# Optimization experiments

Hardware: AMD Instinct MI355X
Metric: run time of the kernel (lower is better)

## Reference

```python
import jax, jax.numpy as jnp
import numpy as np

# --- config (matches init_kwargs) ---
H = 16          # num_attention_heads
DH = 64         # size_per_head
U = H * DH      # units = 1024
M = 8           # num_memory_slots
L = M + 1       # memory slots + current input row
R = 2 * M + 1   # relative position range
EPS = 1e-6
FORGET_BIAS = 1.0
INPUT_BIAS = 0.0
SCALE = 1.0 / np.sqrt(DH)


def _rel_emb():
    # sinusoidal relative-position embedding table [2M+1, U]
    p = np.arange(-M, M + 1, dtype=np.float64)
    i = np.arange(U)
    expo = np.where(i % 2 == 0, i, i - 1) / U
    ang = p[:, None] / np.power(10000.0, expo)[None, :]
    tab = np.where(i % 2 == 0, np.sin(ang), np.cos(ang))
    return jnp.asarray(tab, dtype=jnp.float32)

REL_EMB = _rel_emb()
# rel index table: idx[q,k] = q - k + M  (replaces one-hot pos_table matmul)
_qi = jnp.arange(L)
REL_IDX = _qi[:, None] - _qi[None, :] + M  # [L, L]


def _hard_sigmoid(x):
    return jnp.clip(0.2 * x + 0.5, 0.0, 1.0)


def _ln(x, g, b):
    m = jnp.mean(x, axis=-1, keepdims=True)
    v = jnp.var(x, axis=-1, keepdims=True)
    return (x - m) * jax.lax.rsqrt(v + EPS) * g + b


def setup_inputs() -> dict:
    key = jax.random.key(0)
    ks = jax.random.split(key, 12)
    B, T, DIN = 32, 128, 1024
    s = 0.02
    return {
        "x": jax.random.normal(ks[0], (B, T, DIN), jnp.float32),
        "input_kernel": jax.random.normal(ks[1], (DIN, U), jnp.float32) * s,
        "input_bias": jnp.zeros((U,), jnp.float32),
        "gate_kernel": jax.random.normal(ks[2], (DIN, 2 * U), jnp.float32) * s,
        "recurrent_kernel": jax.random.normal(ks[3], (U, 2 * U), jnp.float32) * s,
        "recurrent_bias": jnp.zeros((2 * U,), jnp.float32),
        "attention_kernel": jax.random.normal(ks[4], (U, 3 * U), jnp.float32) * s,
        "attention_bias": jnp.zeros((3 * U,), jnp.float32),
        "mlp_kernel": jax.random.normal(ks[5], (U, 2 * U), jnp.float32) * s,
        "mlp_bias": jnp.zeros((2 * U,), jnp.float32),
        "ln_gamma": jnp.ones((2 * U,), jnp.float32),
        "ln_beta": jnp.zeros((2 * U,), jnp.float32),
        "rel_kernel": jax.random.normal(ks[6], (U, U), jnp.float32) * s,
    }


def _forward(x, input_kernel, input_bias, gate_kernel, recurrent_kernel,
             recurrent_bias, attention_kernel, attention_bias, mlp_kernel,
             mlp_bias, ln_gamma, ln_beta, rel_kernel):
    B = x.shape[0]
    # relative key projection, shared across steps: [R, H, DH]
    r = (REL_EMB @ rel_kernel).reshape(R, H, DH)

    def step(mem, xt):
        # xt: [B, DIN]; mem: [B, M, U]
        xp = xt @ input_kernel + input_bias              # [B, U]
        mp = jnp.concatenate([mem, xp[:, None, :]], axis=1)  # [B, L, U]
        qkv = mp @ attention_kernel + attention_bias     # [B, L, 3U]
        q, k, v = jnp.split(qkv, 3, axis=-1)
        q = q.reshape(B, L, H, DH).transpose(0, 2, 1, 3)  # [B,H,L,DH]
        k = k.reshape(B, L, H, DH).transpose(0, 2, 1, 3)
        v = v.reshape(B, L, H, DH).transpose(0, 2, 1, 3)
        scores = jnp.einsum('bhqd,bhkd->bhqk', q, k) * SCALE
        rsc = jnp.einsum('bhqd,rhd->bhqr', q, r) * SCALE  # [B,H,L,R]
        scores = scores + rsc[:, :, jnp.arange(L)[:, None], REL_IDX]
        p = jax.nn.softmax(scores, axis=-1)
        attn = jnp.einsum('bhqk,bhkd->bhqd', p, v)
        attn = attn.transpose(0, 2, 1, 3).reshape(B, L, U)
        a1 = _ln(mp + attn, ln_gamma[:U], ln_beta[:U])
        h = jax.nn.gelu(a1 @ mlp_kernel[:, :U] + mlp_bias[:U])
        m2 = h @ mlp_kernel[:, U:] + mlp_bias[U:]
        cand = _ln(a1 + m2, ln_gamma[U:], ln_beta[U:])
        # LSTM-style per-slot gating
        g = (xt @ gate_kernel)[:, None, :] + mp @ recurrent_kernel + recurrent_bias
        ig, fg = jnp.split(g, 2, axis=-1)
        ig = _hard_sigmoid(ig + INPUT_BIAS)
        fg = _hard_sigmoid(fg + FORGET_BIAS)
        nmp = fg * mp + ig * jnp.tanh(cand)              # [B, L, U]
        return nmp[:, :M, :], nmp[:, -1, :]

    mem0 = jnp.zeros((B, M, U), x.dtype)
    _, ys = jax.lax.scan(step, mem0, x.transpose(1, 0, 2))
    return ys.transpose(1, 0, 2)  # [B, T, U]


def reference(x, input_kernel, input_bias, gate_kernel, recurrent_kernel,
              recurrent_bias, attention_kernel, attention_bias, mlp_kernel,
              mlp_bias, ln_gamma, ln_beta, rel_kernel):
    return _forward(x, input_kernel, input_bias, gate_kernel, recurrent_kernel,
                    recurrent_bias, attention_kernel, attention_bias,
                    mlp_kernel, mlp_bias, ln_gamma, ln_beta, rel_kernel)
```

## Files before the change

### kernel.cpp

```cpp
#include <hip/hip_runtime.h>
#include <hip/hip_bf16.h>
#include <math.h>

#define BB 32
#define TT 128
#define UU 1024
#define MM 8
#define LL 9
#define RR 17
#define MROWS 288
#define RSC 4096.0f
#define RSCI (1.0f/4096.0f)

typedef _Float16 f16x8 __attribute__((ext_vector_type(8)));
typedef float f32x4 __attribute__((ext_vector_type(4)));
typedef float f32x8 __attribute__((ext_vector_type(8)));

__device__ __forceinline__ void split2(float v, _Float16* h1, _Float16* h2)
{
    _Float16 a = (_Float16)v;
    float r = (v - (float)a) * RSC;
    *h1 = a; *h2 = (_Float16)r;
}

__device__ __forceinline__ void split2x8(const f32x8 v, f16x8& a, f16x8& b)
{
#pragma unroll
    for (int j = 0; j < 8; ++j) {
        float f = v[j];
        _Float16 h1 = (_Float16)f;
        float r = (f - (float)h1) * RSC;
        a[j] = h1; b[j] = (_Float16)r;
    }
}

__device__ __forceinline__ float gelu_f(float x)
{
    float t = tanhf(0.7978845608028654f * (x + 0.044715f * x * x * x));
    return 0.5f * x * (1.f + t);
}

template<int CG, int NKS, int KLEN>
__global__ __launch_bounds__(256) void gemmks(
    const float* __restrict__ A,
    const _Float16* __restrict__ B1, const _Float16* __restrict__ B2,
    float* __restrict__ P, int N, int GdivP)
{
    static_assert(KLEN % 128 == 0, "pipeline processes chunk pairs");
    int tid = threadIdx.x, wave = tid >> 6, lane = tid & 63;
    int bid = blockIdx.x;
    int x = bid & 7, inner = bid >> 3;
    int q = inner % GdivP, rowT = inner / GdivP;
    int g = x + 8 * q;
    int colT = g / NKS, ks = g % NKS;

    int lr = lane & 15, kg = lane >> 4;
    int row0 = rowT * 32 + (wave & 1) * 16;
    int col0 = colT * (CG * 32) + (wave >> 1) * (CG * 16);
    int kbase = ks * KLEN;

    const float* Ap = A + (size_t)(row0 + lr) * 1024 + kbase + kg * 8;
    size_t boff = (size_t)(col0 + lr) * 1024 + kbase + kg * 8;

    f32x4 accM[CG], accR[CG];
#pragma unroll
    for (int c = 0; c < CG; ++c) {
        accM[c] = (f32x4){0.f, 0.f, 0.f, 0.f};
        accR[c] = (f32x4){0.f, 0.f, 0.f, 0.f};
    }

    f32x8 afA0, afA1, afB0, afB1;
    f16x8 bvA[2][CG][2], bvB[2][CG][2];

    auto loadChunkA = [&](int kc) {
        afA0 = *(const f32x8*)(Ap + kc);
        afA1 = *(const f32x8*)(Ap + kc + 32);
#pragma unroll
        for (int h = 0; h < 2; ++h)
#pragma unroll
            for (int c = 0; c < CG; ++c) {
                size_t o = boff + (size_t)c * 16 * 1024 + kc + h * 32;
                bvA[h][c][0] = *(const f16x8*)(B1 + o);
                bvA[h][c][1] = *(const f16x8*)(B2 + o);
            }
    };
    auto loadChunkB = [&](int kc) {
        afB0 = *(const f32x8*)(Ap + kc);
        afB1 = *(const f32x8*)(Ap + kc + 32);
#pragma unroll
        for (int h = 0; h < 2; ++h)
#pragma unroll
            for (int c = 0; c < CG; ++c) {
                size_t o = boff + (size_t)c * 16 * 1024 + kc + h * 32;
                bvB[h][c][0] = *(const f16x8*)(B1 + o);
                bvB[h][c][1] = *(const f16x8*)(B2 + o);
            }
    };
    auto mfmaChunkA = [&]() {
#pragma unroll
        for (int h = 0; h < 2; ++h) {
            f16x8 a1, a2s;
            split2x8(h ? afA1 : afA0, a1, a2s);
#pragma unroll
            for (int c = 0; c < CG; ++c) {
                accM[c] = __builtin_amdgcn_mfma_f32_16x16x32_f16(a1, bvA[h][c][0], accM[c], 0, 0, 0);
                accR[c] = __builtin_amdgcn_mfma_f32_16x16x32_f16(a1, bvA[h][c][1], accR[c], 0, 0, 0);
                accR[c] = __builtin_amdgcn_mfma_f32_16x16x32_f16(a2s, bvA[h][c][0], accR[c], 0, 0, 0);
            }
        }
    };
    auto mfmaChunkB = [&]() {
#pragma unroll
        for (int h = 0; h < 2; ++h) {
            f16x8 a1, a2s;
            split2x8(h ? afB1 : afB0, a1, a2s);
#pragma unroll
            for (int c = 0; c < CG; ++c) {
                accM[c] = __builtin_amdgcn_mfma_f32_16x16x32_f16(a1, bvB[h][c][0], accM[c], 0, 0, 0);
                accR[c] = __builtin_amdgcn_mfma_f32_16x16x32_f16(a1, bvB[h][c][1], accR[c], 0, 0, 0);
                accR[c] = __builtin_amdgcn_mfma_f32_16x16x32_f16(a2s, bvB[h][c][0], accR[c], 0, 0, 0);
            }
        }
    };

    loadChunkA(0);
#pragma unroll
    for (int kc = 0; kc < KLEN; kc += 128) {
        loadChunkB(kc + 64);
        mfmaChunkA();
        if (kc + 128 < KLEN) loadChunkA(kc + 128);
        mfmaChunkB();
    }

    int r0 = row0 + kg * 4;
    float* Pk = P + (size_t)ks * MROWS * N;
#pragma unroll
    for (int c = 0; c < CG; ++c) {
        int col = col0 + c * 16 + lr;
#pragma unroll
        for (int r = 0; r < 4; ++r)
            Pk[(size_t)(r0 + r) * N + col] = accM[c][r] + accR[c][r] * RSCI;
    }
}

__global__ __launch_bounds__(256) void add4(
    const float* __restrict__ P, const float* __restrict__ bias,
    float* __restrict__ out, int N, int act, int total4)
{
    int idx = blockIdx.x * 256 + threadIdx.x;
    if (idx >= total4) return;
    size_t e = (size_t)idx * 4;
    size_t SP = (size_t)MROWS * N;
    int col = (int)(e % N);
    f32x4 p0 = *(const f32x4*)(P + e);
    f32x4 p1 = *(const f32x4*)(P + SP + e);
    f32x4 p2 = *(const f32x4*)(P + 2 * SP + e);
    f32x4 p3 = *(const f32x4*)(P + 3 * SP + e);
    f32x4 bv = *(const f32x4*)(bias + col);
    f32x4 s;
#pragma unroll
    for (int j = 0; j < 4; ++j) {
        float v = ((p0[j] + p1[j]) + (p2[j] + p3[j])) + bv[j];
        s[j] = act ? gelu_f(v) : v;
    }
    *(f32x4*)(out + e) = s;
}

__global__ __launch_bounds__(256) void gemm2(
    const float* __restrict__ A,
    const _Float16* __restrict__ B1, const _Float16* __restrict__ B2,
    const float* __restrict__ bias, float* __restrict__ C, int ldc, int act)
{
    int wave = threadIdx.x >> 6, lane = threadIdx.x & 63;
    int row0 = blockIdx.y * 32 + (wave >> 1) * 16;
    int col0 = blockIdx.x * 128 + (wave & 1) * 64;
    int lr = lane & 15, kofs = (lane >> 4) * 8;
    const float* Ap = A + (size_t)(row0 + lr) * 1024 + kofs;
    size_t boff = (size_t)(col0 + lr) * 1024 + kofs;
    f32x4 accM[4], accR[4];
#pragma unroll
    for (int c = 0; c < 4; ++c) {
        accM[c] = (f32x4){0.f, 0.f, 0.f, 0.f};
        accR[c] = (f32x4){0.f, 0.f, 0.f, 0.f};
    }
    for (int k = 0; k < 1024; k += 32) {
        f32x8 af = *(const f32x8*)(Ap + k);
        f16x8 a1, a2s;
        split2x8(af, a1, a2s);
#pragma unroll
        for (int c = 0; c < 4; ++c) {
            size_t o = boff + (size_t)c * 16 * 1024 + k;
            f16x8 b1 = *(const f16x8*)(B1 + o);
            f16x8 b2 = *(const f16x8*)(B2 + o);
            accM[c] = __builtin_amdgcn_mfma_f32_16x16x32_f16(a1, b1, accM[c], 0, 0, 0);
            accR[c] = __builtin_amdgcn_mfma_f32_16x16x32_f16(a1, b2, accR[c], 0, 0, 0);
            accR[c] = __builtin_amdgcn_mfma_f32_16x16x32_f16(a2s, b1, accR[c], 0, 0, 0);
        }
    }
    int r0 = row0 + (lane >> 4) * 4;
#pragma unroll
    for (int c = 0; c < 4; ++c) {
        int col = col0 + c * 16 + lr;
        float bv = bias ? bias[col] : 0.f;
#pragma unroll
        for (int r = 0; r < 4; ++r) {
            float v = accM[c][r] + accR[c][r] * RSCI + bv;
            if (act == 1) v = gelu_f(v);
            C[(size_t)(r0 + r) * ldc + col] = v;
        }
    }
}

__global__ __launch_bounds__(256) void transpose_split(
    const float* __restrict__ in,
    _Float16* __restrict__ o1, _Float16* __restrict__ o2, int N)
{
    __shared__ float t[32][33];
    int tx = threadIdx.x & 31, ty = threadIdx.x >> 5;
    int k0 = blockIdx.y * 32, n0 = blockIdx.x * 32;
#pragma unroll
    for (int i = 0; i < 4; ++i)
        t[ty + i * 8][tx] = in[(size_t)(k0 + ty + i * 8) * N + n0 + tx];
    __syncthreads();
#pragma unroll
    for (int i = 0; i < 4; ++i) {
        float v = t[tx][ty + i * 8];
        size_t off = (size_t)(n0 + ty + i * 8) * 1024 + k0 + tx;
        split2(v, o1 + off, o2 + off);
    }
}

#define BKK 16
__global__ __launch_bounds__(256) void gemm_f32(
    const float* __restrict__ A, const float* __restrict__ B,
    float* __restrict__ C, int M, int N, int K)
{
    __shared__ float As[BKK][65];
    __shared__ float Bs[BKK][64];
    int tid = threadIdx.x;
    int row0 = blockIdx.y * 64, col0 = blockIdx.x * 64;
    int ty = tid >> 4, tx = tid & 15;
    float acc[4][4];
#pragma unroll
    for (int i = 0; i < 4; ++i)
#pragma unroll
        for (int j = 0; j < 4; ++j) acc[i][j] = 0.f;
    for (int k0 = 0; k0 < K; k0 += BKK) {
        {
            int r = tid >> 2, kv = (tid & 3) * 4;
            float4 v = make_float4(0.f, 0.f, 0.f, 0.f);
            int gr = row0 + r;
            if (gr < M) v = *(const float4*)(A + (size_t)gr * K + k0 + kv);
            As[kv + 0][r] = v.x; As[kv + 1][r] = v.y;
            As[kv + 2][r] = v.z; As[kv + 3][r] = v.w;
        }
        {
            int r = tid >> 4, cv = (tid & 15) * 4;
            float4 v = *(const float4*)(B + (size_t)(k0 + r) * N + col0 + cv);
            *(float4*)&Bs[r][cv] = v;
        }
        __syncthreads();
#pragma unroll
        for (int kk = 0; kk < BKK; ++kk) {
            float a[4], b[4];
#pragma unroll
            for (int j = 0; j < 4; ++j) a[j] = As[kk][ty * 4 + j];
#pragma unroll
            for (int j = 0; j < 4; ++j) b[j] = Bs[kk][tx * 4 + j];
#pragma unroll
            for (int i = 0; i < 4; ++i)
#pragma unroll
                for (int j = 0; j < 4; ++j) acc[i][j] += a[i] * b[j];
        }
        __syncthreads();
    }
#pragma unroll
    for (int i = 0; i < 4; ++i) {
        int gr = row0 + ty * 4 + i;
        if (gr >= M) continue;
#pragma unroll
        for (int j = 0; j < 4; ++j)
            C[(size_t)gr * N + col0 + tx * 4 + j] = acc[i][j];
    }
}

__global__ void relemb_kernel(float* __restrict__ tab)
{
    int p = blockIdx.x;
    float pv = (float)(p - MM);
    for (int i = threadIdx.x; i < UU; i += blockDim.x) {
        float expo = (float)(i & ~1) * (1.0f / (float)UU);
        float scale = exp2f(-expo * 13.287712379549449f);
        float ang = pv * scale;
        tab[p * UU + i] = (i & 1) ? cosf(ang) : sinf(ang);
    }
}

__global__ void init_mp(const float* __restrict__ xp_all, float* __restrict__ mp)
{
    int row = blockIdx.x;
    int b = row / LL, l = row % LL;
    for (int u = threadIdx.x; u < UU; u += blockDim.x)
        mp[(size_t)row * UU + u] = (l == MM) ? xp_all[((size_t)b * TT) * UU + u] : 0.f;
}

__global__ __launch_bounds__(512) void attn_ln(
    const float* __restrict__ qkvg, const float* __restrict__ rproj,
    const float* __restrict__ mp,
    const float* __restrict__ gamma, const float* __restrict__ beta,
    float* __restrict__ a1)
{
    __shared__ float sA[LL][UU];
    __shared__ float red[16];
    int b = blockIdx.x;
    int tid = threadIdx.x;
    int wave = tid >> 6, lane = tid & 63;

    for (int hh = 0; hh < 2; ++hh) {
        int h = wave + hh * 8;
        const float* base = qkvg + (size_t)b * LL * 5120 + h * 64 + lane;
        float q[LL], k[LL], v[LL], r[RR];
#pragma unroll
        for (int l = 0; l < LL; ++l) {
            q[l] = base[l * 5120];
            k[l] = base[l * 5120 + 1024];
            v[l] = base[l * 5120 + 2048];
        }
#pragma unroll
        for (int rp = 0; rp < RR; ++rp) r[rp] = rproj[rp * UU + h * 64 + lane];
#pragma unroll
        for (int qr = 0; qr < LL; ++qr) {
            float sc[LL];
#pragma unroll
            for (int kr = 0; kr < LL; ++kr) {
                float prod = q[qr] * (k[kr] + r[qr - kr + MM]);
#pragma unroll
                for (int o = 32; o > 0; o >>= 1) prod += __shfl_xor(prod, o);
                sc[kr] = prod * 0.125f;
            }
            float m = sc[0];
#pragma unroll
            for (int kr = 1; kr < LL; ++kr) m = fmaxf(m, sc[kr]);
            float s = 0.f;
#pragma unroll
            for (int kr = 0; kr < LL; ++kr) { sc[kr] = expf(sc[kr] - m); s += sc[kr]; }
            float inv = 1.0f / s;
            float acc = 0.f;
#pragma unroll
            for (int kr = 0; kr < LL; ++kr) acc += sc[kr] * v[kr];
            sA[qr][h * 64 + lane] = acc * inv;
        }
    }
    __syncthreads();

    for (int l = 0; l < LL; ++l) {
        size_t row = (size_t)(b * LL + l);
        float x0 = mp[row * UU + tid] + sA[l][tid];
        float x1 = mp[row * UU + tid + 512] + sA[l][tid + 512];
        float s = x0 + x1, ss = x0 * x0 + x1 * x1;
#pragma unroll
        for (int o = 32; o > 0; o >>= 1) { s += __shfl_xor(s, o); ss += __shfl_xor(ss, o); }
        if (lane == 0) { red[wave * 2] = s; red[wave * 2 + 1] = ss; }
        __syncthreads();
        float S = 0.f, SS = 0.f;
#pragma unroll
        for (int w = 0; w < 8; ++w) { S += red[w * 2]; SS += red[w * 2 + 1]; }
        __syncthreads();
        float mean = S * (1.0f / UU);
        float var = SS * (1.0f / UU) - mean * mean;
        float rstd = rsqrtf(var + 1e-6f);
        a1[row * UU + tid]       = (x0 - mean) * rstd * gamma[tid] + beta[tid];
        a1[row * UU + tid + 512] = (x1 - mean) * rstd * gamma[tid + 512] + beta[tid + 512];
    }
}

__global__ __launch_bounds__(256) void finalize_step(
    const float* __restrict__ a1, const float* __restrict__ m2P,
    const float* __restrict__ bm,
    const float* __restrict__ qkvg, const float* __restrict__ gx_all,
    const float* __restrict__ xp_all,
    const float* __restrict__ gamma, const float* __restrict__ beta,
    float* __restrict__ mp, float* __restrict__ out, int t)
{
    __shared__ float red[8];
    int row = blockIdx.x;
    int b = row / LL, l = row % LL;
    int tid = threadIdx.x;
    int wave = tid >> 6, lane = tid & 63;
    const size_t SP = (size_t)MROWS * UU;

    float x[4];
    float s = 0.f, ss = 0.f;
#pragma unroll
    for (int j = 0; j < 4; ++j) {
        int u = tid + j * 256;
        size_t off = (size_t)row * UU + u;
        float m2v = ((m2P[off] + m2P[SP + off]) + (m2P[2 * SP + off] + m2P[3 * SP + off]))
                    + bm[1024 + u];
        x[j] = a1[off] + m2v;
        s += x[j]; ss += x[j] * x[j];
    }
#pragma unroll
    for (int o = 32; o > 0; o >>= 1) { s += __shfl_xor(s, o); ss += __shfl_xor(ss, o); }
    if (lane == 0) { red[wave * 2] = s; red[wave * 2 + 1] = ss; }
    __syncthreads();
    float S = 0.f, SS = 0.f;
#pragma unroll
    for (int w = 0; w < 4; ++w) { S += red[w * 2]; SS += red[w * 2 + 1]; }
    float mean = S * (1.0f / UU);
    float rstd = rsqrtf(SS * (1.0f / UU) - mean * mean + 1e-6f);

    size_t gxoff = ((size_t)b * TT + t) * 2048;
    size_t grow = (size_t)row * 5120 + 3072;
#pragma unroll
    for (int j = 0; j < 4; ++j) {
        int u = tid + j * 256;
        float cand = (x[j] - mean) * rstd * gamma[1024 + u] + beta[1024 + u];
        float tc = tanhf(cand);
        float gi = gx_all[gxoff + u]        + qkvg[grow + u];
        float gf = gx_all[gxoff + 1024 + u] + qkvg[grow + 1024 + u];
        float ig = fminf(fmaxf(0.2f * gi + 0.5f, 0.f), 1.f);
        float fg = fminf(fmaxf(0.2f * (gf + 1.0f) + 0.5f, 0.f), 1.f);
        size_t off = (size_t)row * UU + u;
        float nmp = fg * mp[off] + ig * tc;
        if (l < MM) {
            mp[off] = nmp;
        } else {
            out[((size_t)b * TT + t) * UU + u] = nmp;
            if (t + 1 < TT)
                mp[off] = xp_all[((size_t)b * TT + t + 1) * UU + u];
        }
    }
}

extern "C" void kernel_launch(void* const* d_in, const int* in_sizes, int n_in,
                              void* d_out, int out_size, void* d_ws, size_t ws_size,
                              hipStream_t stream)
{
    const float* x    = (const float*)d_in[0];
    const float* Wi   = (const float*)d_in[1];
    const float* bi   = (const float*)d_in[2];
    const float* Wg   = (const float*)d_in[3];
    const float* Wr   = (const float*)d_in[4];
    const float* br   = (const float*)d_in[5];
    const float* Wa   = (const float*)d_in[6];
    const float* ba   = (const float*)d_in[7];
    const float* Wm   = (const float*)d_in[8];
    const float* bm   = (const float*)d_in[9];
    const float* gam  = (const float*)d_in[10];
    const float* bet  = (const float*)d_in[11];
    const float* Wrel = (const float*)d_in[12];
    float* out = (float*)d_out;

    char* w = (char*)d_ws;
    float*  xp_all = (float*)w;  w += (size_t)BB*TT*UU*4;
    float*  gx_all = (float*)w;  w += (size_t)BB*TT*2048*4;
    size_t W1N = (size_t)5120 * 1024, WMN = (size_t)2048 * 1024;
    _Float16* W1a = (_Float16*)w;  w += W1N*2;
    _Float16* W1b = (_Float16*)w;  w += W1N*2;
    _Float16* Wma = (_Float16*)w;  w += WMN*2;
    _Float16* Wmb = (_Float16*)w;  w += WMN*2;
    float*  b1    = (float*)w;   w += 5120*4;
    float*  tab   = (float*)w;   w += RR*UU*4;
    float*  rproj = (float*)w;   w += RR*UU*4;
    float*  mp    = (float*)w;   w += (size_t)MROWS*UU*4;
    float*  qkvg  = (float*)w;   w += (size_t)MROWS*5120*4;
    float*  a1    = (float*)w;   w += (size_t)MROWS*UU*4;
    float*  hbuf  = (float*)w;   w += (size_t)MROWS*UU*4;
    char* sbase = w;
    float*  qkvgP = (float*)w;   w += (size_t)4*MROWS*5120*4;
    float*  m1P   = (float*)w;   w += (size_t)4*MROWS*UU*4;
    float*  m2P   = (float*)w;   w += (size_t)4*MROWS*UU*4;
    _Float16* Wia = (_Float16*)sbase;
    _Float16* Wib = Wia + (size_t)1024 * 1024;
    _Float16* Wga = Wib + (size_t)1024 * 1024;
    _Float16* Wgb = Wga + (size_t)2048 * 1024;

    relemb_kernel<<<RR, 256, 0, stream>>>(tab);
    gemm_f32<<<dim3(UU / 64, 1), 256, 0, stream>>>(tab, Wrel, rproj, RR, UU, UU);
    transpose_split<<<dim3(3072 / 32, 32), 256, 0, stream>>>(Wa, W1a, W1b, 3072);
    transpose_split<<<dim3(2048 / 32, 32), 256, 0, stream>>>(
        Wr, W1a + (size_t)3072 * 1024, W1b + (size_t)3072 * 1024, 2048);
    transpose_split<<<dim3(2048 / 32, 32), 256, 0, stream>>>(Wm, Wma, Wmb, 2048);
    transpose_split<<<dim3(1024 / 32, 32), 256, 0, stream>>>(Wi, Wia, Wib, 1024);
    transpose_split<<<dim3(2048 / 32, 32), 256, 0, stream>>>(Wg, Wga, Wgb, 2048);
    hipMemcpyAsync(b1, ba, 3072 * sizeof(float), hipMemcpyDeviceToDevice, stream);
    hipMemcpyAsync(b1 + 3072, br, 2048 * sizeof(float), hipMemcpyDeviceToDevice, stream);
    gemm2<<<dim3(UU / 128, (BB * TT) / 32), 256, 0, stream>>>(
        x, Wia, Wib, bi, xp_all, UU, 0);
    gemm2<<<dim3(2048 / 128, (BB * TT) / 32), 256, 0, stream>>>(
        x, Wga, Wgb, nullptr, gx_all, 2048, 0);
    init_mp<<<MROWS, 256, 0, stream>>>(xp_all, mp);

    for (int t = 0; t < TT; ++t) {
        gemmks<2, 4, 256><<<2880, 256, 0, stream>>>(mp, W1a, W1b, qkvgP, 5120, 40);
        add4<<<(MROWS * 5120 / 4 + 255) / 256, 256, 0, stream>>>(
            qkvgP, b1, qkvg, 5120, 0, MROWS * 5120 / 4);
        attn_ln<<<BB, 512, 0, stream>>>(qkvg, rproj, mp, gam, bet, a1);
        gemmks<2, 4, 256><<<576, 256, 0, stream>>>(a1, Wma, Wmb, m1P, UU, 8);
        add4<<<(MROWS * UU / 4 + 255) / 256, 256, 0, stream>>>(
            m1P, bm, hbuf, UU, 1, MROWS * UU / 4);
        gemmks<2, 4, 256><<<576, 256, 0, stream>>>(hbuf, Wma + (size_t)1024 * 1024,
                                                   Wmb + (size_t)1024 * 1024, m2P, UU, 8);
        finalize_step<<<MROWS, 256, 0, stream>>>(a1, m2P, bm, qkvg, gx_all, xp_all,
                                                 gam, bet, mp, out, t);
    }
}
```

Before: 20.95 ms.

## Fuse split-K reduction and GELU into second MLP GEMM; trim qkv reduction

New measurement: 22.78 ms. 1.09x slower.

```diff
diff --git a/kernel.cpp b/kernel.cpp
--- a/kernel.cpp
+++ b/kernel.cpp
@@ -143,27 +143,106 @@
     }
 }
 
-__global__ __launch_bounds__(256) void add4(
+template<int CG, int NKS, int KLEN>
+__global__ __launch_bounds__(256) void gemmks_af(
+    const float* __restrict__ A,
+    const _Float16* __restrict__ B1, const _Float16* __restrict__ B2,
+    const float* __restrict__ abias,
+    float* __restrict__ P, int N, int GdivP)
+{
+    int tid = threadIdx.x, wave = tid >> 6, lane = tid & 63;
+    int bid = blockIdx.x;
+    int x = bid & 7, inner = bid >> 3;
+    int q = inner % GdivP, rowT = inner / GdivP;
+    int g = x + 8 * q;
+    int colT = g / NKS, ks = g % NKS;
+
+    int lr = lane & 15, kg = lane >> 4;
+    int row0 = rowT * 32 + (wave & 1) * 16;
+    int col0 = colT * (CG * 32) + (wave >> 1) * (CG * 16);
+    int kbase = ks * KLEN;
+
+    const float* Ap = A + (size_t)(row0 + lr) * 1024 + kbase + kg * 8;
+    const float* bp = abias + kbase + kg * 8;
+    const size_t SPA = (size_t)MROWS * 1024;
+    size_t boff = (size_t)(col0 + lr) * 1024 + kbase + kg * 8;
+
+    f32x4 accM[CG], accR[CG];
+#pragma unroll
+    for (int c = 0; c < CG; ++c) {
+        accM[c] = (f32x4){0.f, 0.f, 0.f, 0.f};
+        accR[c] = (f32x4){0.f, 0.f, 0.f, 0.f};
+    }
+
+    for (int kc = 0; kc < KLEN; kc += 64) {
+        f32x8 p00 = *(const f32x8*)(Ap + kc);
+        f32x8 p01 = *(const f32x8*)(Ap + SPA + kc);
+        f32x8 p02 = *(const f32x8*)(Ap + 2 * SPA + kc);
+        f32x8 p03 = *(const f32x8*)(Ap + 3 * SPA + kc);
+        f32x8 p10 = *(const f32x8*)(Ap + kc + 32);
+        f32x8 p11 = *(const f32x8*)(Ap + SPA + kc + 32);
+        f32x8 p12 = *(const f32x8*)(Ap + 2 * SPA + kc + 32);
+        f32x8 p13 = *(const f32x8*)(Ap + 3 * SPA + kc + 32);
+        f32x8 bv0 = *(const f32x8*)(bp + kc);
+        f32x8 bv1 = *(const f32x8*)(bp + kc + 32);
+        f32x8 af0, af1;
+#pragma unroll
+        for (int j = 0; j < 8; ++j) {
+            af0[j] = gelu_f(((p00[j] + p01[j]) + (p02[j] + p03[j])) + bv0[j]);
+            af1[j] = gelu_f(((p10[j] + p11[j]) + (p12[j] + p13[j])) + bv1[j]);
+        }
+        f16x8 bv[2][CG][2];
+#pragma unroll
+        for (int h = 0; h < 2; ++h)
+#pragma unroll
+            for (int c = 0; c < CG; ++c) {
+                size_t o = boff + (size_t)c * 16 * 1024 + kc + h * 32;
+                bv[h][c][0] = *(const f16x8*)(B1 + o);
+                bv[h][c][1] = *(const f16x8*)(B2 + o);
+            }
+#pragma unroll
+        for (int h = 0; h < 2; ++h) {
+            f16x8 a1, a2s;
+            split2x8(h ? af1 : af0, a1, a2s);
+#pragma unroll
+            for (int c = 0; c < CG; ++c) {
+                accM[c] = __builtin_amdgcn_mfma_f32_16x16x32_f16(a1, bv[h][c][0], accM[c], 0, 0, 0);
+                accR[c] = __builtin_amdgcn_mfma_f32_16x16x32_f16(a1, bv[h][c][1], accR[c], 0, 0, 0);
+                accR[c] = __builtin_amdgcn_mfma_f32_16x16x32_f16(a2s, bv[h][c][0], accR[c], 0, 0, 0);
+            }
+        }
+    }
+
+    int r0 = row0 + kg * 4;
+    float* Pk = P + (size_t)ks * MROWS * N;
+#pragma unroll
+    for (int c = 0; c < CG; ++c) {
+        int col = col0 + c * 16 + lr;
+#pragma unroll
+        for (int r = 0; r < 4; ++r)
+            Pk[(size_t)(r0 + r) * N + col] = accM[c][r] + accR[c][r] * RSCI;
+    }
+}
+
+__global__ __launch_bounds__(256) void add4q(
     const float* __restrict__ P, const float* __restrict__ bias,
-    float* __restrict__ out, int N, int act, int total4)
+    float* __restrict__ out)
 {
     int idx = blockIdx.x * 256 + threadIdx.x;
-    if (idx >= total4) return;
-    size_t e = (size_t)idx * 4;
-    size_t SP = (size_t)MROWS * N;
-    int col = (int)(e % N);
+    if (idx >= MROWS * 3072 / 4) return;
+    int row = idx / 768, cq = (idx % 768) * 4;
+    size_t SP = (size_t)MROWS * 5120;
+    size_t e = (size_t)row * 5120 + cq;
     f32x4 p0 = *(const f32x4*)(P + e);
     f32x4 p1 = *(const f32x4*)(P + SP + e);
     f32x4 p2 = *(const f32x4*)(P + 2 * SP + e);
     f32x4 p3 = *(const f32x4*)(P + 3 * SP + e);
-    f32x4 bv = *(const f32x4*)(bias + col);
+    f32x4 bv = *(const f32x4*)(bias + cq);
     f32x4 s;
 #pragma unroll
-    for (int j = 0; j < 4; ++j) {
-        float v = ((p0[j] + p1[j]) + (p2[j] + p3[j])) + bv[j];
-        s[j] = act ? gelu_f(v) : v;
-    }
-    *(f32x4*)(out + e) = s;
+    for (int j = 0; j < 4; ++j)
+        s[j] = ((p0[j] + p1[j]) + (p2[j] + p3[j])) + bv[j];
+    *(f32x4*)(out + (size_t)row * 3072 + cq) = s;
 }
 
 __global__ __launch_bounds__(256) void gemm2(
@@ -305,7 +384,7 @@
 }
 
 __global__ __launch_bounds__(512) void attn_ln(
-    const float* __restrict__ qkvg, const float* __restrict__ rproj,
+    const float* __restrict__ qkvgC, const float* __restrict__ rproj,
     const float* __restrict__ mp,
     const float* __restrict__ gamma, const float* __restrict__ beta,
     float* __restrict__ a1)
@@ -318,13 +397,13 @@
 
     for (int hh = 0; hh < 2; ++hh) {
         int h = wave + hh * 8;
-        const float* base = qkvg + (size_t)b * LL * 5120 + h * 64 + lane;
+        const float* base = qkvgC + (size_t)b * LL * 3072 + h * 64 + lane;
         float q[LL], k[LL], v[LL], r[RR];
 #pragma unroll
         for (int l = 0; l < LL; ++l) {
-            q[l] = base[l * 5120];
-            k[l] = base[l * 5120 + 1024];
-            v[l] = base[l * 5120 + 2048];
+            q[l] = base[l * 3072];
+            k[l] = base[l * 3072 + 1024];
+            v[l] = base[l * 3072 + 2048];
         }
 #pragma unroll
         for (int rp = 0; rp < RR; ++rp) r[rp] = rproj[rp * UU + h * 64 + lane];
@@ -377,7 +456,8 @@
 __global__ __launch_bounds__(256) void finalize_step(
     const float* __restrict__ a1, const float* __restrict__ m2P,
     const float* __restrict__ bm,
-    const float* __restrict__ qkvg, const float* __restrict__ gx_all,
+    const float* __restrict__ qkvgP, const float* __restrict__ b1,
+    const float* __restrict__ gx_all,
     const float* __restrict__ xp_all,
     const float* __restrict__ gamma, const float* __restrict__ beta,
     float* __restrict__ mp, float* __restrict__ out, int t)
@@ -388,6 +468,7 @@
     int tid = threadIdx.x;
     int wave = tid >> 6, lane = tid & 63;
     const size_t SP = (size_t)MROWS * UU;
+    const size_t SPA = (size_t)MROWS * 5120;
 
     float x[4];
     float s = 0.f, ss = 0.f;
@@ -417,8 +498,14 @@
         int u = tid + j * 256;
         float cand = (x[j] - mean) * rstd * gamma[1024 + u] + beta[1024 + u];
         float tc = tanhf(cand);
-        float gi = gx_all[gxoff + u]        + qkvg[grow + u];
-        float gf = gx_all[gxoff + 1024 + u] + qkvg[grow + 1024 + u];
+        float qgi = ((qkvgP[grow + u] + qkvgP[SPA + grow + u])
+                     + (qkvgP[2 * SPA + grow + u] + qkvgP[3 * SPA + grow + u]))
+                    + b1[3072 + u];
+        float qgf = ((qkvgP[grow + 1024 + u] + qkvgP[SPA + grow + 1024 + u])
+                     + (qkvgP[2 * SPA + grow + 1024 + u] + qkvgP[3 * SPA + grow + 1024 + u]))
+                    + b1[4096 + u];
+        float gi = gx_all[gxoff + u]        + qgi;
+        float gf = gx_all[gxoff + 1024 + u] + qgf;
         float ig = fminf(fmaxf(0.2f * gi + 0.5f, 0.f), 1.f);
         float fg = fminf(fmaxf(0.2f * (gf + 1.0f) + 0.5f, 0.f), 1.f);
         size_t off = (size_t)row * UU + u;
@@ -464,9 +551,8 @@
     float*  tab   = (float*)w;   w += RR*UU*4;
     float*  rproj = (float*)w;   w += RR*UU*4;
     float*  mp    = (float*)w;   w += (size_t)MROWS*UU*4;
-    float*  qkvg  = (float*)w;   w += (size_t)MROWS*5120*4;
     float*  a1    = (float*)w;   w += (size_t)MROWS*UU*4;
-    float*  hbuf  = (float*)w;   w += (size_t)MROWS*UU*4;
+    float*  qkvgC = (float*)w;   w += (size_t)MROWS*3072*4;
     char* sbase = w;
     float*  qkvgP = (float*)w;   w += (size_t)4*MROWS*5120*4;
     float*  m1P   = (float*)w;   w += (size_t)4*MROWS*UU*4;
@@ -494,15 +580,13 @@
 
     for (int t = 0; t < TT; ++t) {
         gemmks<2, 4, 256><<<2880, 256, 0, stream>>>(mp, W1a, W1b, qkvgP, 5120, 40);
-        add4<<<(MROWS * 5120 / 4 + 255) / 256, 256, 0, stream>>>(
-            qkvgP, b1, qkvg, 5120, 0, MROWS * 5120 / 4);
-        attn_ln<<<BB, 512, 0, stream>>>(qkvg, rproj, mp, gam, bet, a1);
+        add4q<<<864, 256, 0, stream>>>(qkvgP, b1, qkvgC);
+        attn_ln<<<BB, 512, 0, stream>>>(qkvgC, rproj, mp, gam, bet, a1);
         gemmks<2, 4, 256><<<576, 256, 0, stream>>>(a1, Wma, Wmb, m1P, UU, 8);
-        add4<<<(MROWS * UU / 4 + 255) / 256, 256, 0, stream>>>(
-            m1P, bm, hbuf, UU, 1, MROWS * UU / 4);
-        gemmks<2, 4, 256><<<576, 256, 0, stream>>>(hbuf, Wma + (size_t)1024 * 1024,
-                                                   Wmb + (size_t)1024 * 1024, m2P, UU, 8);
-        finalize_step<<<MROWS, 256, 0, stream>>>(a1, m2P, bm, qkvg, gx_all, xp_all,
-                                                 gam, bet, mp, out, t);
-    }
-}
+        gemmks_af<2, 4, 256><<<576, 256, 0, stream>>>(
+            m1P, Wma + (size_t)1024 * 1024, Wmb + (size_t)1024 * 1024, bm,
+            m2P, UU, 8);
+        finalize_step<<<MROWS, 256, 0, stream>>>(a1, m2P, bm, qkvgP, b1, gx_all,
+                                                 xp_all, gam, bet, mp, out, t);
+    }
+}
```
